# Kernel tuning notes

Measured on AMD Instinct MI355X. Metric: run time of the kernel, lower is better.

Reference implementation:

```python
import jax, jax.numpy as jnp
import numpy as np

# Real spherical harmonics up to l=3 (16 components), standard Condon-Shortley-free
# real SH constants, evaluated on unit vectors (the fused kernel consumes edge
# direction vectors; we normalize as e3nn-style SH kernels do).

def real_sh_l3(vec):
    # vec: [E, 3] -> Y: [E, 16]
    r = jnp.sqrt(jnp.sum(vec * vec, axis=-1, keepdims=True))
    v = vec / jnp.maximum(r, jnp.asarray(1e-12, vec.dtype))
    x, y, z = v[:, 0], v[:, 1], v[:, 2]
    x2, y2, z2 = x * x, y * y, z * z
    C0 = 0.28209479177387814
    C1 = 0.4886025119029199
    Y = [
        jnp.full_like(x, C0),                       # l=0
        C1 * y, C1 * z, C1 * x,                      # l=1 (m=-1,0,1)
        1.0925484305920792 * x * y,                  # l=2, m=-2
        1.0925484305920792 * y * z,                  # l=2, m=-1
        0.31539156525252005 * (3.0 * z2 - 1.0),      # l=2, m=0
        1.0925484305920792 * x * z,                  # l=2, m=1
        0.5462742152960396 * (x2 - y2),              # l=2, m=2
        0.5900435899266435 * y * (3.0 * x2 - y2),    # l=3, m=-3
        2.890611442640554 * x * y * z,               # l=3, m=-2
        0.4570457994644658 * y * (5.0 * z2 - 1.0),   # l=3, m=-1
        0.3731763325901154 * z * (5.0 * z2 - 3.0),   # l=3, m=0
        0.4570457994644658 * x * (5.0 * z2 - 1.0),   # l=3, m=1
        1.445305721320277 * z * (x2 - y2),           # l=3, m=2
        0.5900435899266435 * x * (x2 - 3.0 * y2),    # l=3, m=3
    ]
    return jnp.stack(Y, axis=-1)


def setup_inputs() -> dict:
    key = jax.random.key(0)
    k1, k2, k3, k4, k5 = jax.random.split(key, 5)
    n_atoms, hidden, num_irreps, out_ch = 50000, 32, 16, 32
    n_edges = 800000
    node_features = jax.random.normal(k1, (n_atoms, hidden), dtype=jnp.float32)
    edge_vectors = jax.random.normal(k2, (n_edges, 3), dtype=jnp.float32)
    edge_index = jax.random.randint(k3, (2, n_edges), 0, n_atoms, dtype=jnp.int64)
    fan_in = hidden * num_irreps  # 512
    W = jax.random.normal(k4, (fan_in, out_ch), dtype=jnp.float32) / np.sqrt(fan_in)
    b = jax.random.normal(k5, (out_ch,), dtype=jnp.float32) * 0.01
    return {"node_features": node_features, "edge_vectors": edge_vectors,
            "edge_index": edge_index, "W": W, "b": b}


def reference(node_features, edge_vectors, edge_index, W, b):
    n_atoms = node_features.shape[0]
    sources, targets = edge_index[0], edge_index[1]
    Y = real_sh_l3(edge_vectors)                                  # [E, 16]
    # fused SH + tensor-product: outer product of gathered features with Y
    msg = node_features[sources][:, :, None] * Y[:, None, :]      # [E, C, 16]
    agg = jax.ops.segment_sum(msg, targets, num_segments=n_atoms) # [N, C, 16]
    out = agg.reshape(n_atoms, -1) @ W + b                        # [N, out]
    return out
```

## Files before the change

kernel.cpp:

```cpp
#include <hip/hip_runtime.h>
#include <hip/hip_bf16.h>
#include <hip/hip_fp16.h>


#define HIDDEN 32
#define IRREPS 16
#define OUTCH  32
#define CAP    48
#define WPB    16
#define AGP    584
#define GCAP   8192
#define C0SH   0.28209479177387814f

typedef __attribute__((ext_vector_type(8))) short frag8;
typedef __attribute__((ext_vector_type(4))) float f32x4;
typedef __attribute__((ext_vector_type(4))) unsigned int u32x4v;

__device__ __forceinline__ unsigned short bf16bits(float f) {
    __hip_bfloat16 t = __float2bfloat16(f);
    return *(unsigned short*)&t;
}
__device__ __forceinline__ unsigned short f16bits(float f) {
    __half h = __float2half(f);
    return *(unsigned short*)&h;
}
__device__ __forceinline__ float f16tof(unsigned short u) {
    __half h = *(__half*)&u;
    return __half2float(h);
}
__device__ __forceinline__ frag8 mkfrag(unsigned a, unsigned b, unsigned c, unsigned d) {
    u32x4v v = {a, b, c, d};
    return __builtin_bit_cast(frag8, v);
}

__global__ __launch_bounds__(256)
void zero_repack_kernel(const float* __restrict__ W,
                        const float* __restrict__ nf,
                        int* __restrict__ gcursor,
                        __hip_bfloat162* __restrict__ nfb2,
                        __hip_bfloat16* __restrict__ w2frag, int n_atoms) {
    const int tid = blockIdx.x * blockDim.x + threadIdx.x;
    const int gsz = gridDim.x * blockDim.x;
    if (tid < 256) gcursor[tid] = 0;
    const float2* nf2 = (const float2*)nf;
    const int total2 = n_atoms * (HIDDEN / 2);
    for (int i = tid; i < total2; i += gsz) {
        const float2 t = nf2[i];
        __hip_bfloat162 p;
        p.x = __float2bfloat16(t.x);
        p.y = __float2bfloat16(t.y);
        nfb2[i] = p;
    }
    if (tid < 2048) {
        const int lane = tid & 63;
        const int kk   = tid >> 7;
        const int n    = (((tid >> 6) & 1) << 4) + (lane & 15);
        const int kb   = kk * 32 + (lane >> 4) * 8;
#pragma unroll
        for (int j = 0; j < 8; ++j)
            w2frag[tid * 8 + j] = __float2bfloat16(W[(kb + j) * OUTCH + n]);
    }
}

__global__ __launch_bounds__(256)
void split_kernel(const float* __restrict__ ev,
                  const int* __restrict__ ei,
                  int* __restrict__ gcursor,
                  uint4* __restrict__ gbuf,
                  int n_edges) {
    __shared__ int hist[256];
    __shared__ int cur[256];
    const int e0 = blockIdx.x * 2048 + threadIdx.x * 8;
    hist[threadIdx.x] = 0;
    __syncthreads();

    int   sr[8], tg[8];
    float vx[8], vy[8], vz[8];
    const int cnt = min(max(n_edges - e0, 0), 8);
    if (cnt == 8 && (n_edges & 3) == 0) {
        const int4 s0 = *(const int4*)(ei + e0);
        const int4 s1 = *(const int4*)(ei + e0 + 4);
        const int4 t0 = *(const int4*)(ei + n_edges + e0);
        const int4 t1 = *(const int4*)(ei + n_edges + e0 + 4);
        sr[0]=s0.x; sr[1]=s0.y; sr[2]=s0.z; sr[3]=s0.w;
        sr[4]=s1.x; sr[5]=s1.y; sr[6]=s1.z; sr[7]=s1.w;
        tg[0]=t0.x; tg[1]=t0.y; tg[2]=t0.z; tg[3]=t0.w;
        tg[4]=t1.x; tg[5]=t1.y; tg[6]=t1.z; tg[7]=t1.w;
        const float4* e4 = (const float4*)(ev + 3 * e0);
        float f[24];
#pragma unroll
        for (int q = 0; q < 6; ++q) {
            const float4 v = e4[q];
            f[q*4+0]=v.x; f[q*4+1]=v.y; f[q*4+2]=v.z; f[q*4+3]=v.w;
        }
#pragma unroll
        for (int j = 0; j < 8; ++j) { vx[j]=f[3*j]; vy[j]=f[3*j+1]; vz[j]=f[3*j+2]; }
    } else {
        for (int j = 0; j < cnt; ++j) {
            const int e = e0 + j;
            sr[j] = ei[e];
            tg[j] = ei[n_edges + e];
            vx[j] = ev[3*e]; vy[j] = ev[3*e+1]; vz[j] = ev[3*e+2];
        }
    }

    for (int j = 0; j < cnt; ++j) atomicAdd(&hist[tg[j] >> 8], 1);
    __syncthreads();
    {
        const int h = hist[threadIdx.x];
        cur[threadIdx.x] = h ? atomicAdd(&gcursor[threadIdx.x], h) : 0;
    }
    __syncthreads();

    for (int j = 0; j < cnt; ++j) {
        const int g = tg[j] >> 8;
        const int pos = atomicAdd(&cur[g], 1);
        if (pos >= GCAP) continue;
        const float rinv = 1.0f /
            fmaxf(sqrtf(vx[j]*vx[j] + vy[j]*vy[j] + vz[j]*vz[j]), 1e-12f);
        uint4 r;
        r.x = (unsigned)(sr[j] & 0xffff) | ((unsigned)f16bits(vx[j]*rinv) << 16);
        r.y = (unsigned)f16bits(vy[j]*rinv) | ((unsigned)f16bits(vz[j]*rinv) << 16);
        r.z = (unsigned)tg[j];
        r.w = 0u;
        gbuf[(size_t)g * GCAP + pos] = r;
    }
}

__global__ __launch_bounds__(1024)
void bucket_kernel(const uint4* __restrict__ gbuf,
                   const int* __restrict__ gcursor,
                   uint2* __restrict__ recs,
                   int* __restrict__ cursor,
                   int n_atoms) {
    __shared__ int lcur[256];
    const int g = blockIdx.x;
    if (threadIdx.x < 256) lcur[threadIdx.x] = 0;
    __syncthreads();
    const int n = min(gcursor[g], GCAP);
    const uint4* gb = gbuf + (size_t)g * GCAP;
    for (int i = threadIdx.x; i < n; i += 1024) {
        const uint4 r = gb[i];
        const int tgt = (int)r.z;
        const int slot = atomicAdd(&lcur[tgt & 255], 1);
        if (slot < CAP) {
            uint2 d; d.x = r.x; d.y = r.y;
            recs[(size_t)tgt * CAP + slot] = d;
        }
    }
    __syncthreads();
    const int a = g * 256 + threadIdx.x;
    if (threadIdx.x < 256 && a < n_atoms)
        cursor[a] = lcur[threadIdx.x];
}

__global__ __launch_bounds__(1024, 8)
void acc_gemm_kernel(const uint2* __restrict__ recs,
                     const int* __restrict__ cursor,
                     const __hip_bfloat16* __restrict__ nfb,
                     const __hip_bfloat16* __restrict__ w2frag,
                     const float* __restrict__ bias,
                     float* __restrict__ out,
                     int n_atoms) {
    __shared__ short ldsY[WPB][64 * 18];
    __shared__ short ldsAgg[WPB][AGP];
    __shared__ int   ldsS[WPB][64];
    const int wv   = threadIdx.x >> 6;
    const int lane = threadIdx.x & 63;
    const int w    = min(blockIdx.x * WPB + wv, n_atoms - 1);

    const int k = min(max(__builtin_amdgcn_readfirstlane(cursor[w]), 0), CAP);

    {
        float Yv[16];
#pragma unroll
        for (int q = 0; q < 16; ++q) Yv[q] = 0.f;
        int s = 0;
        if (lane < k) {
            const uint2 rec = recs[(size_t)w * CAP + lane];
            s = (int)(rec.x & 0xffffu);
            const float x = f16tof((unsigned short)(rec.x >> 16));
            const float y = f16tof((unsigned short)(rec.y & 0xffffu));
            const float z = f16tof((unsigned short)(rec.y >> 16));
            const float x2 = x * x, y2 = y * y, z2 = z * z;
            const float xy = x * y, yz = y * z, xz = x * z;
            const float xmy = x2 - y2;
            const float fz2 = fmaf(5.0f, z2, -1.0f);
            Yv[0]  = C0SH;
            Yv[1]  = 0.4886025119029199f * y;
            Yv[2]  = 0.4886025119029199f * z;
            Yv[3]  = 0.4886025119029199f * x;
            Yv[4]  = 1.0925484305920792f * xy;
            Yv[5]  = 1.0925484305920792f * yz;
            Yv[6]  = 0.31539156525252005f * fmaf(3.0f, z2, -1.0f);
            Yv[7]  = 1.0925484305920792f * xz;
            Yv[8]  = 0.5462742152960396f * xmy;
            Yv[9]  = 0.5900435899266435f * y * fmaf(2.0f, x2, xmy);
            Yv[10] = 2.890611442640554f * xy * z;
            Yv[11] = 0.4570457994644658f * y * fz2;
            Yv[12] = 0.3731763325901154f * z * fmaf(5.0f, z2, -3.0f);
            Yv[13] = 0.4570457994644658f * x * fz2;
            Yv[14] = 1.445305721320277f * z * xmy;
            Yv[15] = 0.5900435899266435f * x * fmaf(-3.0f, y2, x2);
        }
        ldsS[wv][lane] = s;
        short* yr = &ldsY[wv][lane * 18];
#pragma unroll
        for (int d = 0; d < 8; ++d)
            *(unsigned*)&yr[d * 2] =
                (unsigned)bf16bits(Yv[2 * d]) | ((unsigned)bf16bits(Yv[2 * d + 1]) << 16);
    }
    asm volatile("s_waitcnt lgkmcnt(0)" ::: "memory");
    __builtin_amdgcn_sched_barrier(0);

    const int kq = lane >> 4;
    const int m  = lane & 15;
    f32x4 acc0 = {0.f, 0.f, 0.f, 0.f};
    f32x4 acc1 = {0.f, 0.f, 0.f, 0.f};
    {
        const short* yrow = &ldsY[wv][0];
        const int* sv = &ldsS[wv][0];
        const unsigned short* nfu = (const unsigned short*)nfb;
        const int nks = (k > 32) ? 2 : 1;
        for (int ks = 0; ks < nks; ++ks) {
            const int e0 = ks * 32 + kq * 8;
            int sj[8];
#pragma unroll
            for (int j = 0; j < 8; ++j) sj[j] = sv[e0 + j];
            unsigned bu[4], au0[4], au1[4];
#pragma unroll
            for (int p = 0; p < 4; ++p) {
                const unsigned ylo = *(const unsigned short*)&yrow[(e0 + 2 * p) * 18 + m];
                const unsigned yhi = *(const unsigned short*)&yrow[(e0 + 2 * p + 1) * 18 + m];
                bu[p] = ylo | (yhi << 16);
                const unsigned short* r0 = nfu + sj[2 * p] * HIDDEN + m;
                const unsigned short* r1 = nfu + sj[2 * p + 1] * HIDDEN + m;
                const unsigned a00 = r0[0], a01 = r1[0];
                au0[p] = a00 | (a01 << 16);
                const unsigned a10 = r0[16], a11 = r1[16];
                au1[p] = a10 | (a11 << 16);
            }
            const frag8 bf = mkfrag(bu[0], bu[1], bu[2], bu[3]);
            acc0 = __builtin_amdgcn_mfma_f32_16x16x32_bf16(
                mkfrag(au0[0], au0[1], au0[2], au0[3]), bf, acc0, 0, 0, 0);
            acc1 = __builtin_amdgcn_mfma_f32_16x16x32_bf16(
                mkfrag(au1[0], au1[1], au1[2], au1[3]), bf, acc1, 0, 0, 0);
        }
    }

    {
        short* arow = &ldsAgg[wv][0];
#pragma unroll
        for (int r = 0; r < 4; ++r) {
            arow[kq * 72 + r * 16 + m]       = (short)bf16bits(acc0[r]);
            arow[kq * 72 + r * 16 + m + 288] = (short)bf16bits(acc1[r]);
        }
    }

    __syncthreads();

    if (wv < 2) {
        const int m2   = lane & 15;
        const int quad = lane >> 4;
        const int nh   = wv;
        const short* wf = (const short*)w2frag;
        f32x4 acc = {0.f, 0.f, 0.f, 0.f};
#pragma unroll
        for (int kk = 0; kk < 16; ++kk) {
            const int sidx = kk * 32 + quad * 8 + (kk >> 1) * 8;
            frag8 a  = *(const frag8*)&ldsAgg[m2][sidx];
            frag8 bb = *(const frag8*)(wf + ((kk * 2 + nh) * 64 + lane) * 8);
            acc = __builtin_amdgcn_mfma_f32_16x16x32_bf16(a, bb, acc, 0, 0, 0);
        }
        const float bi = bias[nh * 16 + m2];
        const int tile0 = blockIdx.x * WPB;
#pragma unroll
        for (int r = 0; r < 4; ++r) {
            const int row = tile0 + quad * 4 + r;
            if (row < n_atoms)
                out[(size_t)row * OUTCH + nh * 16 + m2] = acc[r] + bi;
        }
    }
}

extern "C" void kernel_launch(void* const* d_in, const int* in_sizes, int n_in,
                              void* d_out, int out_size, void* d_ws, size_t ws_size,
                              hipStream_t stream) {
    const float* nf = (const float*)d_in[0];
    const float* ev = (const float*)d_in[1];
    const int*   ei = (const int*)d_in[2];
    const float* W  = (const float*)d_in[3];
    const float* b  = (const float*)d_in[4];
    float* out = (float*)d_out;

    const int n_atoms = in_sizes[0] / HIDDEN;
    const int n_edges = in_sizes[1] / 3;
    const int ngroups = (n_atoms + 255) >> 8;

    char* ws = (char*)d_ws;
    size_t off = 0;
    auto carve = [&](size_t bytes) { void* p = ws + off; off = (off + bytes + 255) & ~(size_t)255; return p; };
    uint2*           recs    = (uint2*)carve((size_t)n_atoms * CAP * 8);
    uint4*           gbuf    = (uint4*)carve((size_t)ngroups * GCAP * 16);
    __hip_bfloat162* nfb2    = (__hip_bfloat162*)carve((size_t)n_atoms * HIDDEN * 2);
    __hip_bfloat16*  w2frag  = (__hip_bfloat16*)carve(2048 * 8 * 2);
    int*             cursor  = (int*)carve((size_t)n_atoms * 4);
    int*             gcursor = (int*)carve(256 * 4);

    zero_repack_kernel<<<512, 256, 0, stream>>>(W, nf, gcursor, nfb2, w2frag, n_atoms);

    const int sblocks = (n_edges + 2047) / 2048;
    split_kernel<<<sblocks, 256, 0, stream>>>(ev, ei, gcursor, gbuf, n_edges);

    bucket_kernel<<<ngroups, 1024, 0, stream>>>(gbuf, gcursor, recs, cursor, n_atoms);

    const int blocks3 = (n_atoms + WPB - 1) / WPB;
    acc_gemm_kernel<<<blocks3, WPB * 64, 0, stream>>>(
        recs, cursor, (const __hip_bfloat16*)nfb2, w2frag, b, out, n_atoms);
}
```

Before: 60.18 us.

## Interleave bf16 node features into paired dwords and pad group cursors

Repacks node features so that channel m and channel m+16 share one 32-bit word. Each gathered source row then needs 8 dword loads per lane instead of 32 short loads, and the two MFMA A-fragments are assembled by shifts and masks. Separately, the per-group atomic cursors are spread out with a stride of 16 ints to reduce atomic contention and false sharing between neighbouring groups. The repack kernel now issues vectorized float4 reads and uint4 writes.

```diff
diff --git a/kernel.cpp b/kernel.cpp
--- a/kernel.cpp
+++ b/kernel.cpp
@@ -10,6 +10,7 @@
 #define WPB    16
 #define AGP    584
 #define GCAP   8192
+#define GSTR   16
 #define C0SH   0.28209479177387814f
 
 typedef __attribute__((ext_vector_type(8))) short frag8;
@@ -37,19 +38,22 @@
 void zero_repack_kernel(const float* __restrict__ W,
                         const float* __restrict__ nf,
                         int* __restrict__ gcursor,
-                        __hip_bfloat162* __restrict__ nfb2,
+                        unsigned* __restrict__ nfT,
                         __hip_bfloat16* __restrict__ w2frag, int n_atoms) {
     const int tid = blockIdx.x * blockDim.x + threadIdx.x;
     const int gsz = gridDim.x * blockDim.x;
-    if (tid < 256) gcursor[tid] = 0;
-    const float2* nf2 = (const float2*)nf;
-    const int total2 = n_atoms * (HIDDEN / 2);
-    for (int i = tid; i < total2; i += gsz) {
-        const float2 t = nf2[i];
-        __hip_bfloat162 p;
-        p.x = __float2bfloat16(t.x);
-        p.y = __float2bfloat16(t.y);
-        nfb2[i] = p;
+    if (tid < 256 * GSTR) gcursor[tid] = 0;
+    const int tq = n_atoms * 4;
+    for (int i = tid; i < tq; i += gsz) {
+        const int s = i >> 2, q = (i & 3) * 4;
+        const float4 lo = *(const float4*)(nf + s * HIDDEN + q);
+        const float4 hi = *(const float4*)(nf + s * HIDDEN + 16 + q);
+        uint4 o;
+        o.x = (unsigned)bf16bits(lo.x) | ((unsigned)bf16bits(hi.x) << 16);
+        o.y = (unsigned)bf16bits(lo.y) | ((unsigned)bf16bits(hi.y) << 16);
+        o.z = (unsigned)bf16bits(lo.z) | ((unsigned)bf16bits(hi.z) << 16);
+        o.w = (unsigned)bf16bits(lo.w) | ((unsigned)bf16bits(hi.w) << 16);
+        *(uint4*)(nfT + s * 16 + q) = o;
     }
     if (tid < 2048) {
         const int lane = tid & 63;
@@ -108,7 +112,7 @@
     __syncthreads();
     {
         const int h = hist[threadIdx.x];
-        cur[threadIdx.x] = h ? atomicAdd(&gcursor[threadIdx.x], h) : 0;
+        cur[threadIdx.x] = h ? atomicAdd(&gcursor[threadIdx.x * GSTR], h) : 0;
     }
     __syncthreads();
 
@@ -137,7 +141,7 @@
     const int g = blockIdx.x;
     if (threadIdx.x < 256) lcur[threadIdx.x] = 0;
     __syncthreads();
-    const int n = min(gcursor[g], GCAP);
+    const int n = min(gcursor[g * GSTR], GCAP);
     const uint4* gb = gbuf + (size_t)g * GCAP;
     for (int i = threadIdx.x; i < n; i += 1024) {
         const uint4 r = gb[i];
@@ -157,7 +161,7 @@
 __global__ __launch_bounds__(1024, 8)
 void acc_gemm_kernel(const uint2* __restrict__ recs,
                      const int* __restrict__ cursor,
-                     const __hip_bfloat16* __restrict__ nfb,
+                     const unsigned* __restrict__ nfT,
                      const __hip_bfloat16* __restrict__ w2frag,
                      const float* __restrict__ bias,
                      float* __restrict__ out,
@@ -203,7 +207,7 @@
             Yv[14] = 1.445305721320277f * z * xmy;
             Yv[15] = 0.5900435899266435f * x * fmaf(-3.0f, y2, x2);
         }
-        ldsS[wv][lane] = s;
+        ldsS[wv][lane] = s << 4;
         short* yr = &ldsY[wv][lane * 18];
 #pragma unroll
         for (int d = 0; d < 8; ++d)
@@ -220,25 +224,22 @@
     {
         const short* yrow = &ldsY[wv][0];
         const int* sv = &ldsS[wv][0];
-        const unsigned short* nfu = (const unsigned short*)nfb;
         const int nks = (k > 32) ? 2 : 1;
         for (int ks = 0; ks < nks; ++ks) {
             const int e0 = ks * 32 + kq * 8;
-            int sj[8];
-#pragma unroll
-            for (int j = 0; j < 8; ++j) sj[j] = sv[e0 + j];
+            unsigned g[8];
+#pragma unroll
+            for (int j = 0; j < 8; ++j)
+                g[j] = nfT[sv[e0 + j] + m];
             unsigned bu[4], au0[4], au1[4];
 #pragma unroll
             for (int p = 0; p < 4; ++p) {
                 const unsigned ylo = *(const unsigned short*)&yrow[(e0 + 2 * p) * 18 + m];
                 const unsigned yhi = *(const unsigned short*)&yrow[(e0 + 2 * p + 1) * 18 + m];
                 bu[p] = ylo | (yhi << 16);
-                const unsigned short* r0 = nfu + sj[2 * p] * HIDDEN + m;
-                const unsigned short* r1 = nfu + sj[2 * p + 1] * HIDDEN + m;
-                const unsigned a00 = r0[0], a01 = r1[0];
-                au0[p] = a00 | (a01 << 16);
-                const unsigned a10 = r0[16], a11 = r1[16];
-                au1[p] = a10 | (a11 << 16);
+                const unsigned g0 = g[2 * p], g1 = g[2 * p + 1];
+                au0[p] = (g0 & 0xffffu) | (g1 << 16);
+                au1[p] = (g0 >> 16) | (g1 & 0xffff0000u);
             }
             const frag8 bf = mkfrag(bu[0], bu[1], bu[2], bu[3]);
             acc0 = __builtin_amdgcn_mfma_f32_16x16x32_bf16(
@@ -300,14 +301,14 @@
     char* ws = (char*)d_ws;
     size_t off = 0;
     auto carve = [&](size_t bytes) { void* p = ws + off; off = (off + bytes + 255) & ~(size_t)255; return p; };
-    uint2*           recs    = (uint2*)carve((size_t)n_atoms * CAP * 8);
-    uint4*           gbuf    = (uint4*)carve((size_t)ngroups * GCAP * 16);
-    __hip_bfloat162* nfb2    = (__hip_bfloat162*)carve((size_t)n_atoms * HIDDEN * 2);
-    __hip_bfloat16*  w2frag  = (__hip_bfloat16*)carve(2048 * 8 * 2);
-    int*             cursor  = (int*)carve((size_t)n_atoms * 4);
-    int*             gcursor = (int*)carve(256 * 4);
-
-    zero_repack_kernel<<<512, 256, 0, stream>>>(W, nf, gcursor, nfb2, w2frag, n_atoms);
+    uint2*          recs    = (uint2*)carve((size_t)n_atoms * CAP * 8);
+    uint4*          gbuf    = (uint4*)carve((size_t)ngroups * GCAP * 16);
+    unsigned*       nfT     = (unsigned*)carve((size_t)n_atoms * 16 * 4);
+    __hip_bfloat16* w2frag  = (__hip_bfloat16*)carve(2048 * 8 * 2);
+    int*            cursor  = (int*)carve((size_t)n_atoms * 4);
+    int*            gcursor = (int*)carve(256 * GSTR * 4);
+
+    zero_repack_kernel<<<512, 256, 0, stream>>>(W, nf, gcursor, nfT, w2frag, n_atoms);
 
     const int sblocks = (n_edges + 2047) / 2048;
     split_kernel<<<sblocks, 256, 0, stream>>>(ev, ei, gcursor, gbuf, n_edges);
@@ -316,5 +317,5 @@
 
     const int blocks3 = (n_atoms + WPB - 1) / WPB;
     acc_gemm_kernel<<<blocks3, WPB * 64, 0, stream>>>(
-        recs, cursor, (const __hip_bfloat16*)nfb2, w2frag, b, out, n_atoms);
-}
+        recs, cursor, nfT, w2frag, b, out, n_atoms);
+}
```

After: 58.91 us. 1.02x faster.
